# Kernel optimization log

Measured on AMD Instinct MI355X. Metric: run time of the kernel, lower is better.

Reference implementation:

```python
import jax, jax.numpy as jnp
import numpy as np

T, B, D, E, H = 64, 1024, 128, 256, 512


def _gru(x_emb, h0, W_ih, W_hh, b_ih, b_hh):
    """Standard GRU (PyTorch gate convention) over time-major x_emb [T,B,E]."""
    xW = x_emb @ W_ih + b_ih  # [T,B,3H], precompute input contractions

    def step(h, xw):
        hW = h @ W_hh + b_hh
        xr, xz, xn = jnp.split(xw, 3, axis=-1)
        hr, hz, hn = jnp.split(hW, 3, axis=-1)
        r = jax.nn.sigmoid(xr + hr)
        z = jax.nn.sigmoid(xz + hz)
        n = jnp.tanh(xn + r * hn)
        h_new = (1.0 - z) * n + z * h
        return h_new, h_new

    h_t, ys = jax.lax.scan(step, h0, xW)
    return ys, h_t


def setup_inputs() -> dict:
    key = jax.random.key(0)
    ks = jax.random.split(key, 16)
    s_in = 1.0 / np.sqrt(D)
    s_emb = 1.0 / np.sqrt(E)
    s_hid = 1.0 / np.sqrt(H)
    return {
        "past_input": jax.random.normal(ks[0], (T, B, D), jnp.float32),
        "future_input": jax.random.normal(ks[1], (T, B, D), jnp.float32),
        "noise": jax.random.normal(ks[2], (B, H), jnp.float32),
        "W_emb": jax.random.normal(ks[3], (D, E), jnp.float32) * s_in,
        "b_emb": jnp.zeros((E,), jnp.float32),
        "W_ih_enc": jax.random.normal(ks[4], (E, 3 * H), jnp.float32) * s_emb,
        "W_hh_enc": jax.random.normal(ks[5], (H, 3 * H), jnp.float32) * s_hid,
        "b_ih_enc": jnp.zeros((3 * H,), jnp.float32),
        "b_hh_enc": jnp.zeros((3 * H,), jnp.float32),
        "W_ih_dec": jax.random.normal(ks[6], (E, 3 * H), jnp.float32) * s_emb,
        "W_hh_dec": jax.random.normal(ks[7], (H, 3 * H), jnp.float32) * s_hid,
        "b_ih_dec": jnp.zeros((3 * H,), jnp.float32),
        "b_hh_dec": jnp.zeros((3 * H,), jnp.float32),
        "W_out": jax.random.normal(ks[8], (H, D), jnp.float32) * s_hid,
        "b_out": jnp.zeros((D,), jnp.float32),
    }


def reference(past_input, future_input, noise, W_emb, b_emb,
              W_ih_enc, W_hh_enc, b_ih_enc, b_hh_enc,
              W_ih_dec, W_hh_dec, b_ih_dec, b_hh_dec,
              W_out, b_out):
    past_emb = jax.nn.relu(past_input @ W_emb + b_emb)      # [T,B,E]
    fut_emb = jax.nn.relu(future_input @ W_emb + b_emb)     # [T,B,E]

    h0 = jnp.zeros((past_emb.shape[1], W_hh_enc.shape[0]), past_emb.dtype)
    _, h_t = _gru(past_emb, h0, W_ih_enc, W_hh_enc, b_ih_enc, b_hh_enc)

    # shift future embedding: step 0 -> zeros, step t -> emb at t-1
    fut_shift = jnp.concatenate([jnp.zeros_like(fut_emb[:1]), fut_emb[:-1]], axis=0)

    hidden = h_t + noise
    future_target, _ = _gru(fut_shift, hidden, W_ih_dec, W_hh_dec, b_ih_dec, b_hh_dec)
    return future_target @ W_out + b_out  # [T,B,D]
```

## Files before the change

### kernel.cpp

```cpp
#include <hip/hip_runtime.h>

typedef __bf16 bf16;
typedef __bf16 bf16x8 __attribute__((ext_vector_type(8)));
typedef float f32x4 __attribute__((ext_vector_type(4)));

#define Tt 64
#define Bb 1024
#define Dd 128
#define Ee 256
#define Hh 512
#define H3 1536

__device__ __forceinline__ float sigmf(float x) { return 1.0f / (1.0f + __expf(-x)); }
__device__ __forceinline__ float tanhfast(float x) {
    float e = __expf(2.0f * x);
    return 1.0f - 2.0f / (e + 1.0f);
}

#define LD_SC(dst, bp, OFF) \
    asm volatile("global_load_dwordx4 %0, %1, off offset:" #OFF " sc0 sc1" : "=v"(dst) : "v"(bp))
#define ST_SC(bp, OFF, val) \
    asm volatile("global_store_short %0, %1, off offset:" #OFF " sc0 sc1" :: "v"(bp), "v"(val))
#define LDROW16(arr, bp) \
    LD_SC(arr[0], bp, 0);    LD_SC(arr[1], bp, 64);   LD_SC(arr[2], bp, 128);  LD_SC(arr[3], bp, 192);  \
    LD_SC(arr[4], bp, 256);  LD_SC(arr[5], bp, 320);  LD_SC(arr[6], bp, 384);  LD_SC(arr[7], bp, 448);  \
    LD_SC(arr[8], bp, 512);  LD_SC(arr[9], bp, 576);  LD_SC(arr[10], bp, 640); LD_SC(arr[11], bp, 704); \
    LD_SC(arr[12], bp, 768); LD_SC(arr[13], bp, 832); LD_SC(arr[14], bp, 896); LD_SC(arr[15], bp, 960);

__global__ void k_prep(const float* __restrict__ We, const float* __restrict__ Wie, const float* __restrict__ Whe,
                       const float* __restrict__ Wid, const float* __restrict__ Whd, const float* __restrict__ Wo,
                       bf16* __restrict__ dWe, bf16* __restrict__ dWie, bf16* __restrict__ dWhe,
                       bf16* __restrict__ dWid, bf16* __restrict__ dWhd, bf16* __restrict__ dWo) {
    long i = (long)blockIdx.x * 256 + threadIdx.x;
    const float* s;
    bf16* d;
    int K, N;
    if (i < 32768) { s = We; d = dWe; K = Dd; N = Ee; }
    else if ((i -= 32768) < 393216) { s = Wie; d = dWie; K = Ee; N = H3; }
    else if ((i -= 393216) < 786432) { s = Whe; d = dWhe; K = Hh; N = H3; }
    else if ((i -= 786432) < 393216) { s = Wid; d = dWid; K = Ee; N = H3; }
    else if ((i -= 393216) < 786432) { s = Whd; d = dWhd; K = Hh; N = H3; }
    else if ((i -= 786432) < 65536) { s = Wo; d = dWo; K = Hh; N = Dd; }
    else return;
    int n = (int)(i / K), k = (int)(i - (long)n * K);
    d[i] = (bf16)s[(size_t)k * N + n];
}

__global__ __launch_bounds__(256) void k_embed(const float* __restrict__ xP, const float* __restrict__ xF,
                                               const bf16* __restrict__ WT, const float* __restrict__ bias,
                                               bf16* __restrict__ oP, bf16* __restrict__ oF) {
    const int lane = threadIdx.x & 63, wv = threadIdx.x >> 6;
    const float* x = blockIdx.z ? xF : xP;
    bf16* o = blockIdx.z ? oF : oP;
    const int m0w = blockIdx.x * 128 + wv * 32;
    const int c0 = blockIdx.y * 64;
    const int koff = (lane >> 4) * 8;
    f32x4 acc[2][4];
#pragma unroll
    for (int m = 0; m < 2; ++m)
#pragma unroll
        for (int s = 0; s < 4; ++s) acc[m][s] = f32x4{0.f, 0.f, 0.f, 0.f};

    const float* xp0 = x + (size_t)(m0w + (lane & 15)) * Dd + koff;
#pragma unroll
    for (int kc = 0; kc < 4; ++kc) {
        bf16x8 a0, a1;
        {
            float4 f0 = *(const float4*)(xp0 + kc * 32);
            float4 f1 = *(const float4*)(xp0 + kc * 32 + 4);
            a0[0] = (bf16)f0.x; a0[1] = (bf16)f0.y; a0[2] = (bf16)f0.z; a0[3] = (bf16)f0.w;
            a0[4] = (bf16)f1.x; a0[5] = (bf16)f1.y; a0[6] = (bf16)f1.z; a0[7] = (bf16)f1.w;
            float4 g0 = *(const float4*)(xp0 + 16 * Dd + kc * 32);
            float4 g1 = *(const float4*)(xp0 + 16 * Dd + kc * 32 + 4);
            a1[0] = (bf16)g0.x; a1[1] = (bf16)g0.y; a1[2] = (bf16)g0.z; a1[3] = (bf16)g0.w;
            a1[4] = (bf16)g1.x; a1[5] = (bf16)g1.y; a1[6] = (bf16)g1.z; a1[7] = (bf16)g1.w;
        }
#pragma unroll
        for (int s = 0; s < 4; ++s) {
            bf16x8 b = *(const bf16x8*)(WT + (size_t)(c0 + s * 16 + (lane & 15)) * Dd + kc * 32 + koff);
            acc[0][s] = __builtin_amdgcn_mfma_f32_16x16x32_bf16(a0, b, acc[0][s], 0, 0, 0);
            acc[1][s] = __builtin_amdgcn_mfma_f32_16x16x32_bf16(a1, b, acc[1][s], 0, 0, 0);
        }
    }
#pragma unroll
    for (int m = 0; m < 2; ++m)
#pragma unroll
        for (int s = 0; s < 4; ++s) {
            int col = c0 + s * 16 + (lane & 15);
            float bv = bias[col];
#pragma unroll
            for (int r = 0; r < 4; ++r) {
                int row = m0w + m * 16 + (lane >> 4) * 4 + r;
                o[(size_t)row * Ee + col] = (bf16)fmaxf(acc[m][s][r] + bv, 0.0f);
            }
        }
}

__global__ __launch_bounds__(512, 1) void k_gru_all(
    const bf16* __restrict__ embP, const bf16* __restrict__ embF, const float* __restrict__ noise,
    const bf16* __restrict__ WihE, const bf16* __restrict__ WhhE,
    const float* __restrict__ bIhE, const float* __restrict__ bHhE,
    const bf16* __restrict__ WihD, const bf16* __restrict__ WhhD,
    const float* __restrict__ bIhD, const float* __restrict__ bHhD,
    bf16* __restrict__ hA, bf16* __restrict__ hB, bf16* __restrict__ ys, unsigned* __restrict__ flags) {
    __shared__ bf16 Wih[6 * 8 * 64 * 8];
    __shared__ bf16 Whh[6 * 16 * 64 * 8];
    const int tid = threadIdx.x;
    const int lane = tid & 63, wv = tid >> 6;
    const int im = blockIdx.x >> 4;
    const int in = blockIdx.x & 15;
    const int rh = wv >> 1, ch = wv & 1;
    const int rowb = im * 64 + rh * 16;
    const int arow0 = rowb + (lane & 15);
    const int koff = (lane >> 4) * 8;
    const int colc = in * 32 + ch * 16 + (lane & 15);

    const bf16x8* WihV = (const bf16x8*)Wih;
    const bf16x8* WhhV = (const bf16x8*)Whh;

    auto stage = [&](const bf16* WT, int Kdim, int KC, bf16* lds) {
        int total = 6 * KC * 64;
        for (int idx = tid; idx < total; idx += 512) {
            int ln = idx & 63;
            int kc = (idx >> 6) % KC;
            int s = (idx >> 6) / KC;
            int gate = s >> 1, f = s & 1;
            int col = gate * Hh + in * 32 + f * 16 + (ln & 15);
            int k = kc * 32 + (ln >> 4) * 8;
            *(bf16x8*)(lds + (size_t)idx * 8) = *(const bf16x8*)(WT + (size_t)col * Kdim + k);
        }
    };

    float bi[3], bh[3];
    auto load_bias = [&](const float* bIh, const float* bHh) {
#pragma unroll
        for (int g = 0; g < 3; ++g) {
            bi[g] = bIh[g * Hh + colc];
            bh[g] = bHh[g * Hh + colc];
        }
    };

    auto signal = [&](unsigned seq) {
        asm volatile("s_waitcnt vmcnt(0)" ::: "memory");
        __syncthreads();
        if (tid == 0) {
            unsigned* fp = flags + ((size_t)im * 16 + in) * 16;
            asm volatile("global_store_dword %0, %1, off sc0 sc1" :: "v"(fp), "v"(seq) : "memory");
        }
    };
    auto wait_flags = [&](unsigned seq) {
        const unsigned* fp = flags + ((size_t)im * 16 + (lane & 15)) * 16;
        for (;;) {
            unsigned v;
            asm volatile("global_load_dword %0, %1, off sc0 sc1\n\ts_waitcnt vmcnt(0)"
                         : "=v"(v) : "v"(fp) : "memory");
            if (__all((int)(v >= seq))) break;
            __builtin_amdgcn_s_sleep(1);
        }
    };

    f32x4 aR, aZ, aNX, aNH;
    auto zacc = [&]() {
        aR = f32x4{0.f, 0.f, 0.f, 0.f};
        aZ = f32x4{0.f, 0.f, 0.f, 0.f};
        aNX = f32x4{0.f, 0.f, 0.f, 0.f};
        aNH = f32x4{0.f, 0.f, 0.f, 0.f};
    };

    auto xp_phase = [&](const bf16* xp) {
        const bf16* ap = xp + (size_t)arow0 * Ee + koff;
#pragma unroll
        for (int kc = 0; kc < 8; ++kc) {
            bf16x8 a = *(const bf16x8*)(ap + kc * 32);
            aR = __builtin_amdgcn_mfma_f32_16x16x32_bf16(a, WihV[((0 + ch) * 8 + kc) * 64 + lane], aR, 0, 0, 0);
            aZ = __builtin_amdgcn_mfma_f32_16x16x32_bf16(a, WihV[((2 + ch) * 8 + kc) * 64 + lane], aZ, 0, 0, 0);
            aNX = __builtin_amdgcn_mfma_f32_16x16x32_bf16(a, WihV[((4 + ch) * 8 + kc) * 64 + lane], aNX, 0, 0, 0);
        }
    };

    auto hw_phase = [&](const bf16* hp) {
        const bf16* h0p = hp + (size_t)arow0 * Hh + koff;
        bf16x8 h0[16];
        LDROW16(h0, h0p);
        asm volatile("s_waitcnt vmcnt(0)" ::: "memory");
        __builtin_amdgcn_sched_barrier(0);
#pragma unroll
        for (int kc = 0; kc < 16; ++kc) {
            aR = __builtin_amdgcn_mfma_f32_16x16x32_bf16(h0[kc], WhhV[((0 + ch) * 16 + kc) * 64 + lane], aR, 0, 0, 0);
            aZ = __builtin_amdgcn_mfma_f32_16x16x32_bf16(h0[kc], WhhV[((2 + ch) * 16 + kc) * 64 + lane], aZ, 0, 0, 0);
            aNH = __builtin_amdgcn_mfma_f32_16x16x32_bf16(h0[kc], WhhV[((4 + ch) * 16 + kc) * 64 + lane], aNH, 0, 0, 0);
        }
    };

    float hreg[4];
#pragma unroll
    for (int i = 0; i < 4; ++i) hreg[i] = 0.0f;

    auto epi = [&](bf16* op) {
        bf16* stb = op + (size_t)(rowb + (lane >> 4) * 4) * Hh + colc;
        unsigned short us[4];
#pragma unroll
        for (int r = 0; r < 4; ++r) {
            float rg = sigmf(aR[r] + bi[0] + bh[0]);
            float zg = sigmf(aZ[r] + bi[1] + bh[1]);
            float ng = tanhfast(aNX[r] + bi[2] + rg * (aNH[r] + bh[2]));
            float hv = (1.0f - zg) * ng + zg * hreg[r];
            hreg[r] = hv;
            us[r] = __builtin_bit_cast(unsigned short, (bf16)hv);
        }
        ST_SC(stb, 0, us[0]);
        ST_SC(stb, 1024, us[1]);
        ST_SC(stb, 2048, us[2]);
        ST_SC(stb, 3072, us[3]);
    };

    stage(WihE, Ee, 8, Wih);
    stage(WhhE, Hh, 16, Whh);
    load_bias(bIhE, bHhE);
    __syncthreads();

#pragma unroll 1
    for (int t = 0; t < Tt; ++t) {
        zacc();
        xp_phase(embP + (size_t)t * Bb * Ee);
        if (t > 0) {
            wait_flags((unsigned)t);
            hw_phase(((t - 1) & 1) ? hB : hA);
        }
        epi((t & 1) ? hB : hA);
        signal((unsigned)(t + 1));
    }

    wait_flags((unsigned)Tt);
    {
        bf16* stb = hA + (size_t)(rowb + (lane >> 4) * 4) * Hh + colc;
        unsigned short us[4];
#pragma unroll
        for (int r = 0; r < 4; ++r) {
            int row = rowb + (lane >> 4) * 4 + r;
            float v = hreg[r] + noise[(size_t)row * Hh + colc];
            hreg[r] = v;
            us[r] = __builtin_bit_cast(unsigned short, (bf16)v);
        }
        ST_SC(stb, 0, us[0]);
        ST_SC(stb, 1024, us[1]);
        ST_SC(stb, 2048, us[2]);
        ST_SC(stb, 3072, us[3]);
    }
    stage(WihD, Ee, 8, Wih);
    stage(WhhD, Hh, 16, Whh);
    load_bias(bIhD, bHhD);
    signal((unsigned)(Tt + 1));
    wait_flags((unsigned)(Tt + 1));

#pragma unroll 1
    for (int t = 0; t < Tt; ++t) {
        zacc();
        if (t > 0) {
            xp_phase(embF + (size_t)(t - 1) * Bb * Ee);
            wait_flags((unsigned)(Tt + 1 + t));
        }
        hw_phase(t ? ys + (size_t)(t - 1) * Bb * Hh : hA);
        epi(ys + (size_t)t * Bb * Hh);
        if (t < Tt - 1) signal((unsigned)(Tt + 2 + t));
    }
}

__global__ __launch_bounds__(256) void k_out(const bf16* __restrict__ ys, const bf16* __restrict__ WT,
                                             const float* __restrict__ bias, float* __restrict__ out) {
    const int lane = threadIdx.x & 63, wv = threadIdx.x >> 6;
    const int m0w = blockIdx.x * 256 + wv * 64;
    const int c0 = blockIdx.y * 64;
    const int koff = (lane >> 4) * 8;
    f32x4 acc[4][4];
#pragma unroll
    for (int m = 0; m < 4; ++m)
#pragma unroll
        for (int s = 0; s < 4; ++s) acc[m][s] = f32x4{0.f, 0.f, 0.f, 0.f};

    const bf16* ap = ys + (size_t)(m0w + (lane & 15)) * Hh + koff;
#pragma unroll
    for (int kc = 0; kc < 16; ++kc) {
        bf16x8 a0 = *(const bf16x8*)(ap + kc * 32);
        bf16x8 a1 = *(const bf16x8*)(ap + 16 * Hh + kc * 32);
        bf16x8 a2 = *(const bf16x8*)(ap + 32 * Hh + kc * 32);
        bf16x8 a3 = *(const bf16x8*)(ap + 48 * Hh + kc * 32);
#pragma unroll
        for (int s = 0; s < 4; ++s) {
            bf16x8 b = *(const bf16x8*)(WT + (size_t)(c0 + s * 16 + (lane & 15)) * Hh + kc * 32 + koff);
            acc[0][s] = __builtin_amdgcn_mfma_f32_16x16x32_bf16(a0, b, acc[0][s], 0, 0, 0);
            acc[1][s] = __builtin_amdgcn_mfma_f32_16x16x32_bf16(a1, b, acc[1][s], 0, 0, 0);
            acc[2][s] = __builtin_amdgcn_mfma_f32_16x16x32_bf16(a2, b, acc[2][s], 0, 0, 0);
            acc[3][s] = __builtin_amdgcn_mfma_f32_16x16x32_bf16(a3, b, acc[3][s], 0, 0, 0);
        }
    }
#pragma unroll
    for (int m = 0; m < 4; ++m)
#pragma unroll
        for (int s = 0; s < 4; ++s) {
            int col = c0 + s * 16 + (lane & 15);
            float bv = bias[col];
#pragma unroll
            for (int r = 0; r < 4; ++r) {
                int row = m0w + m * 16 + (lane >> 4) * 4 + r;
                out[(size_t)row * Dd + col] = acc[m][s][r] + bv;
            }
        }
}

extern "C" void kernel_launch(void* const* d_in, const int* in_sizes, int n_in,
                              void* d_out, int out_size, void* d_ws, size_t ws_size,
                              hipStream_t stream) {
    const float* past = (const float*)d_in[0];
    const float* fut = (const float*)d_in[1];
    const float* noise = (const float*)d_in[2];
    const float* W_emb = (const float*)d_in[3];
    const float* b_emb = (const float*)d_in[4];
    const float* W_ih_enc = (const float*)d_in[5];
    const float* W_hh_enc = (const float*)d_in[6];
    const float* b_ih_enc = (const float*)d_in[7];
    const float* b_hh_enc = (const float*)d_in[8];
    const float* W_ih_dec = (const float*)d_in[9];
    const float* W_hh_dec = (const float*)d_in[10];
    const float* b_ih_dec = (const float*)d_in[11];
    const float* b_hh_dec = (const float*)d_in[12];
    const float* W_out = (const float*)d_in[13];
    const float* b_out = (const float*)d_in[14];
    float* out = (float*)d_out;

    char* w = (char*)d_ws;
    auto alloc = [&](size_t bytes) {
        char* p = w;
        w += (bytes + 255) & ~(size_t)255;
        return p;
    };
    bf16* embP = (bf16*)alloc((size_t)Tt * Bb * Ee * 2);
    bf16* embF = (bf16*)alloc((size_t)Tt * Bb * Ee * 2);
    bf16* ys = (bf16*)alloc((size_t)Tt * Bb * Hh * 2);
    bf16* hA = (bf16*)alloc((size_t)Bb * Hh * 2);
    bf16* hB = (bf16*)alloc((size_t)Bb * Hh * 2);
    bf16* WembT = (bf16*)alloc((size_t)Ee * Dd * 2);
    bf16* WihEncT = (bf16*)alloc((size_t)H3 * Ee * 2);
    bf16* WhhEncT = (bf16*)alloc((size_t)H3 * Hh * 2);
    bf16* WihDecT = (bf16*)alloc((size_t)H3 * Ee * 2);
    bf16* WhhDecT = (bf16*)alloc((size_t)H3 * Hh * 2);
    bf16* WoutT = (bf16*)alloc((size_t)Dd * Hh * 2);
    unsigned* flags = (unsigned*)alloc(16 * 16 * 64);

    k_prep<<<9600, 256, 0, stream>>>(W_emb, W_ih_enc, W_hh_enc, W_ih_dec, W_hh_dec, W_out,
                                     WembT, WihEncT, WhhEncT, WihDecT, WhhDecT, WoutT);

    k_embed<<<dim3(Tt * Bb / 128, Ee / 64, 2), 256, 0, stream>>>(past, fut, WembT, b_emb, embP, embF);

    hipMemsetAsync(flags, 0, 16 * 16 * 64, stream);

    void* args[] = {(void*)&embP, (void*)&embF, (void*)&noise,
                    (void*)&WihEncT, (void*)&WhhEncT, (void*)&b_ih_enc, (void*)&b_hh_enc,
                    (void*)&WihDecT, (void*)&WhhDecT, (void*)&b_ih_dec, (void*)&b_hh_dec,
                    (void*)&hA, (void*)&hB, (void*)&ys, (void*)&flags};
    hipLaunchCooperativeKernel((const void*)k_gru_all, dim3(256), dim3(512), args, 0, stream);

    k_out<<<dim3(Tt * Bb / 256, Dd / 64), 256, 0, stream>>>(ys, WoutT, b_out, out);
}
```

Measured before the change: 1.096 ms.

## Use per-wave flags and progressive chunk-wise waits in persistent GRU kernel

Replaces block-level barriers and per-block flags with per-wave flags grouped by 16-row domains, so each wave signals without __syncthreads. The hidden-state load now polls readiness and issues each 32-column K-chunk load as soon as its two producer waves have signalled, overlapping waiting with loading. Block-to-tile mapping is remapped to interleave row groups across block IDs, which changes placement across XCDs. This adds polling traffic and finer-grained memory-ordering risk in exchange for less barrier latency per timestep.

```diff
diff --git a/kernel.cpp b/kernel.cpp
--- a/kernel.cpp
+++ b/kernel.cpp
@@ -21,11 +21,6 @@
     asm volatile("global_load_dwordx4 %0, %1, off offset:" #OFF " sc0 sc1" : "=v"(dst) : "v"(bp))
 #define ST_SC(bp, OFF, val) \
     asm volatile("global_store_short %0, %1, off offset:" #OFF " sc0 sc1" :: "v"(bp), "v"(val))
-#define LDROW16(arr, bp) \
-    LD_SC(arr[0], bp, 0);    LD_SC(arr[1], bp, 64);   LD_SC(arr[2], bp, 128);  LD_SC(arr[3], bp, 192);  \
-    LD_SC(arr[4], bp, 256);  LD_SC(arr[5], bp, 320);  LD_SC(arr[6], bp, 384);  LD_SC(arr[7], bp, 448);  \
-    LD_SC(arr[8], bp, 512);  LD_SC(arr[9], bp, 576);  LD_SC(arr[10], bp, 640); LD_SC(arr[11], bp, 704); \
-    LD_SC(arr[12], bp, 768); LD_SC(arr[13], bp, 832); LD_SC(arr[14], bp, 896); LD_SC(arr[15], bp, 960);
 
 __global__ void k_prep(const float* __restrict__ We, const float* __restrict__ Wie, const float* __restrict__ Whe,
                        const float* __restrict__ Wid, const float* __restrict__ Whd, const float* __restrict__ Wo,
@@ -107,13 +102,16 @@
     __shared__ bf16 Whh[6 * 16 * 64 * 8];
     const int tid = threadIdx.x;
     const int lane = tid & 63, wv = tid >> 6;
-    const int im = blockIdx.x >> 4;
-    const int in = blockIdx.x & 15;
+    const int bid = blockIdx.x;
+    const int im = (bid & 7) * 2 + (bid >> 7);
+    const int in = (bid >> 3) & 15;
     const int rh = wv >> 1, ch = wv & 1;
     const int rowb = im * 64 + rh * 16;
     const int arow0 = rowb + (lane & 15);
     const int koff = (lane >> 4) * 8;
     const int colc = in * 32 + ch * 16 + (lane & 15);
+    unsigned* dom = flags + ((size_t)im * 4 + rh) * 32;
+    const int myidx = in * 2 + ch;
 
     const bf16x8* WihV = (const bf16x8*)Wih;
     const bf16x8* WhhV = (const bf16x8*)Whh;
@@ -142,21 +140,20 @@
 
     auto signal = [&](unsigned seq) {
         asm volatile("s_waitcnt vmcnt(0)" ::: "memory");
-        __syncthreads();
-        if (tid == 0) {
-            unsigned* fp = flags + ((size_t)im * 16 + in) * 16;
+        if (lane == 0) {
+            unsigned* fp = dom + myidx;
             asm volatile("global_store_dword %0, %1, off sc0 sc1" :: "v"(fp), "v"(seq) : "memory");
         }
     };
-    auto wait_flags = [&](unsigned seq) {
-        const unsigned* fp = flags + ((size_t)im * 16 + (lane & 15)) * 16;
-        for (;;) {
-            unsigned v;
-            asm volatile("global_load_dword %0, %1, off sc0 sc1\n\ts_waitcnt vmcnt(0)"
-                         : "=v"(v) : "v"(fp) : "memory");
-            if (__all((int)(v >= seq))) break;
-            __builtin_amdgcn_s_sleep(1);
-        }
+    auto poll = [&](unsigned seq) -> unsigned long long {
+        unsigned v;
+        const unsigned* fp = dom + (lane & 31);
+        asm volatile("global_load_dword %0, %1, off sc0 sc1\n\ts_waitcnt vmcnt(0)"
+                     : "=v"(v) : "v"(fp) : "memory");
+        return __ballot((int)(v >= seq));
+    };
+    auto wait_all = [&](unsigned seq) {
+        while (poll(seq) != ~0ULL) __builtin_amdgcn_s_sleep(2);
     };
 
     f32x4 aR, aZ, aNX, aNH;
@@ -178,10 +175,18 @@
         }
     };
 
-    auto hw_phase = [&](const bf16* hp) {
+    auto hw_phase = [&](const bf16* hp, unsigned seq) {
         const bf16* h0p = hp + (size_t)arow0 * Hh + koff;
         bf16x8 h0[16];
-        LDROW16(h0, h0p);
+        unsigned long long rdy = poll(seq);
+#define HSTEP(p, OFF) \
+        while (((rdy >> (2 * p)) & 3ULL) != 3ULL) { __builtin_amdgcn_s_sleep(2); rdy = poll(seq); } \
+        LD_SC(h0[p], h0p, OFF);
+        HSTEP(0, 0)    HSTEP(1, 64)   HSTEP(2, 128)  HSTEP(3, 192)
+        HSTEP(4, 256)  HSTEP(5, 320)  HSTEP(6, 384)  HSTEP(7, 448)
+        HSTEP(8, 512)  HSTEP(9, 576)  HSTEP(10, 640) HSTEP(11, 704)
+        HSTEP(12, 768) HSTEP(13, 832) HSTEP(14, 896) HSTEP(15, 960)
+#undef HSTEP
         asm volatile("s_waitcnt vmcnt(0)" ::: "memory");
         __builtin_amdgcn_sched_barrier(0);
 #pragma unroll
@@ -223,15 +228,12 @@
     for (int t = 0; t < Tt; ++t) {
         zacc();
         xp_phase(embP + (size_t)t * Bb * Ee);
-        if (t > 0) {
-            wait_flags((unsigned)t);
-            hw_phase(((t - 1) & 1) ? hB : hA);
-        }
+        if (t > 0) hw_phase(((t - 1) & 1) ? hB : hA, (unsigned)t);
         epi((t & 1) ? hB : hA);
         signal((unsigned)(t + 1));
     }
 
-    wait_flags((unsigned)Tt);
+    wait_all((unsigned)Tt);
     {
         bf16* stb = hA + (size_t)(rowb + (lane >> 4) * 4) * Hh + colc;
         unsigned short us[4];
@@ -247,20 +249,18 @@
         ST_SC(stb, 2048, us[2]);
         ST_SC(stb, 3072, us[3]);
     }
+    __syncthreads();
     stage(WihD, Ee, 8, Wih);
     stage(WhhD, Hh, 16, Whh);
+    __syncthreads();
     load_bias(bIhD, bHhD);
     signal((unsigned)(Tt + 1));
-    wait_flags((unsigned)(Tt + 1));
 
 #pragma unroll 1
     for (int t = 0; t < Tt; ++t) {
         zacc();
-        if (t > 0) {
-            xp_phase(embF + (size_t)(t - 1) * Bb * Ee);
-            wait_flags((unsigned)(Tt + 1 + t));
-        }
-        hw_phase(t ? ys + (size_t)(t - 1) * Bb * Hh : hA);
+        if (t > 0) xp_phase(embF + (size_t)(t - 1) * Bb * Ee);
+        hw_phase(t ? ys + (size_t)(t - 1) * Bb * Hh : hA, (unsigned)(Tt + 1 + t));
         epi(ys + (size_t)t * Bb * Hh);
         if (t < Tt - 1) signal((unsigned)(Tt + 2 + t));
     }
@@ -345,14 +345,14 @@
     bf16* WihDecT = (bf16*)alloc((size_t)H3 * Ee * 2);
     bf16* WhhDecT = (bf16*)alloc((size_t)H3 * Hh * 2);
     bf16* WoutT = (bf16*)alloc((size_t)Dd * Hh * 2);
-    unsigned* flags = (unsigned*)alloc(16 * 16 * 64);
+    unsigned* flags = (unsigned*)alloc(16 * 4 * 32 * sizeof(unsigned));
 
     k_prep<<<9600, 256, 0, stream>>>(W_emb, W_ih_enc, W_hh_enc, W_ih_dec, W_hh_dec, W_out,
                                      WembT, WihEncT, WhhEncT, WihDecT, WhhDecT, WoutT);
 
     k_embed<<<dim3(Tt * Bb / 128, Ee / 64, 2), 256, 0, stream>>>(past, fut, WembT, b_emb, embP, embF);
 
-    hipMemsetAsync(flags, 0, 16 * 16 * 64, stream);
+    hipMemsetAsync(flags, 0, 16 * 4 * 32 * sizeof(unsigned), stream);
 
     void* args[] = {(void*)&embP, (void*)&embF, (void*)&noise,
                     (void*)&WihEncT, (void*)&WhhEncT, (void*)&b_ih_enc, (void*)&b_hh_enc,
```

New measurement: 1.069 ms. -2.5%, faster.
